# Optimization experiments

Measured on AMD Instinct MI355X. Metric: run time of the kernel, lower is better.

The kernel has to match this reference:

```python
import jax, jax.numpy as jnp
import numpy as np

N_NODES = 20000
DIM = 128
N_EDGES = 500000
BATCH = 16384
EPS = 1e-6  # torch.nn.PairwiseDistance default eps


def setup_inputs() -> dict:
    key = jax.random.key(0)
    k = jax.random.split(key, 8)
    edges = jax.random.randint(k[0], (2, N_EDGES), 0, N_NODES, dtype=jnp.int64 if jax.config.jax_enable_x64 else jnp.int32)
    nodes_p_star = jnp.sort(jax.random.randint(k[1], (BATCH,), 0, N_NODES))
    nodes_p = jnp.sort(jax.random.randint(k[2], (BATCH,), 0, N_NODES))
    # learned parameters, init in [-1, 1) as in the torch module
    beta_p = 2.0 * jax.random.uniform(k[3], (N_NODES,), dtype=jnp.float32) - 1.0
    beta_p_star = 2.0 * jax.random.uniform(k[4], (N_NODES,), dtype=jnp.float32) - 1.0
    p = 2.0 * jax.random.uniform(k[5], (N_NODES, DIM), dtype=jnp.float32) - 1.0
    p_star = 2.0 * jax.random.uniform(k[6], (N_NODES, DIM), dtype=jnp.float32) - 1.0
    return {
        "edges": edges,
        "nodes_p_star": nodes_p_star,
        "nodes_p": nodes_p,
        "beta_p": beta_p,
        "beta_p_star": beta_p_star,
        "p": p,
        "p_star": p_star,
    }


def reference(edges, nodes_p_star, nodes_p, beta_p, beta_p_star, p, p_star):
    # ---- link term: sum over observed edges of (beta - dist) ----
    beta_pair = beta_p_star[edges[0]] + beta_p[edges[1]]  # [E]
    diff = p[edges[0]] - p_star[edges[1]]                 # [E, D]
    # torch PairwiseDistance adds eps to the difference before the norm
    z_dist = jnp.sqrt(jnp.sum((diff + EPS) ** 2, axis=-1))
    link_term = jnp.sum(beta_pair - z_dist)

    # ---- non-link term: triu-masked sum of exp(beta - cdist) ----
    bps = beta_p_star[nodes_p_star]   # [Ns]
    bp = beta_p[nodes_p]              # [Np]
    ps = p_star[nodes_p_star]         # [Ns, D]
    pp = p[nodes_p]                   # [Np, D]
    beta_mat = bps[None, :] + bp[:, None]          # [Np, Ns]
    # cdist(ps, pp) -> [Ns, Np] via Gram trick
    sq = (jnp.sum(ps * ps, axis=-1)[:, None]
          + jnp.sum(pp * pp, axis=-1)[None, :]
          - 2.0 * jnp.einsum('nd,md->nm', ps, pp))
    dist_mat = jnp.sqrt(jnp.maximum(sq, 0.0))      # [Ns, Np]
    intensity = jnp.exp(beta_mat.T - dist_mat)     # [Ns, Np]
    non_link = jnp.sum(jnp.triu(intensity, k=1))

    return -(link_term - non_link)
```

## Files before the change

kernel.cpp:

```cpp
#include <hip/hip_runtime.h>

#define N_NODES 20000
#define DIM 128
#define N_EDGES 500000
#define BATCH 16384
#define EPS 1e-6f
#define L2E 1.4426950408889634f

typedef _Float16 half8 __attribute__((ext_vector_type(8)));
typedef _Float16 half4_t __attribute__((ext_vector_type(4)));
typedef float f32x4 __attribute__((ext_vector_type(4)));

__device__ __forceinline__ float fast_sqrtf(float x) {
#if __has_builtin(__builtin_amdgcn_sqrtf)
    return __builtin_amdgcn_sqrtf(x);
#else
    return sqrtf(x);
#endif
}
__device__ __forceinline__ float fast_exp2f(float x) {
#if __has_builtin(__builtin_amdgcn_exp2f)
    return __builtin_amdgcn_exp2f(x);
#else
    return exp2f(x);
#endif
}

#define NB_TILE 8256
#define N_BLK   512

#define OFF_PGEMM 0
#define OFF_PSH   33280
#define OFF_PPH   4227584
#define OFF_N2S   8421888
#define OFF_N2P   8487424
#define OFF_BPS   8552960
#define OFF_BP    8618496
#define OFF_END   8684032

__global__ __launch_bounds__(256) void prep_kernel(
    const float* __restrict__ p, const float* __restrict__ p_star,
    const float* __restrict__ beta_p, const float* __restrict__ beta_ps,
    const int* __restrict__ nodes_ps, const int* __restrict__ nodes_p,
    _Float16* __restrict__ Ah, float* __restrict__ n2A, float* __restrict__ bA2,
    _Float16* __restrict__ Bh, float* __restrict__ n2B, float* __restrict__ bB2)
{
    const int bx = blockIdx.x;
    const int g = threadIdx.x & 31;
    const int r8 = threadIdx.x >> 5;
    const bool isA = bx < 2048;
    const int row = (isA ? bx : bx - 2048) * 8 + r8;
    const int id = isA ? nodes_ps[row] : nodes_p[row];
    const float* src = isA ? p_star : p;
    float4 v = ((const float4*)(src + (size_t)id * DIM))[g];
    half4_t o;
    o[0] = (_Float16)v.x; o[1] = (_Float16)v.y; o[2] = (_Float16)v.z; o[3] = (_Float16)v.w;
    const int h = g >> 4;
    const int pc = ((g >> 1) & 7) ^ (row & 7);
    _Float16* dst = isA ? Ah : Bh;
    *(half4_t*)(dst + (size_t)row * DIM + (((h << 3) | pc) << 3) + (g & 1) * 4) = o;
    float nrm = v.x * v.x + v.y * v.y + v.z * v.z + v.w * v.w;
    #pragma unroll
    for (int m = 16; m >= 1; m >>= 1) nrm += __shfl_xor(nrm, m, 32);
    if (g == 0) {
        if (isA) { n2A[row] = nrm; bA2[row] = L2E * beta_ps[id]; }
        else     { n2B[row] = nrm; bB2[row] = L2E * beta_p[id]; }
    }
}

__device__ __forceinline__ void tile_of(int t, int& i0, int& j0, bool& diag) {
    const int by = t / 129;
    const int bx = t - by * 129;
    const int len = 128 - by;
    int ti, tj;
    if (bx < len) { ti = by; tj = by + bx; }
    else          { ti = 127 - by; tj = 127 - (bx - len); }
    i0 = ti << 7; j0 = tj << 7; diag = (ti == tj);
}

#define STAGE(I0, J0)                                                              \
    {                                                                              \
        _Pragma("unroll")                                                          \
        for (int u = 0; u < 4; ++u) {                                              \
            const int cidx = u * 512 + tid;                                        \
            const int row = cidx >> 4, cc = cidx & 15;                             \
            const int ldsoff = (u * 512 + w * 64) * 16;                            \
            __builtin_amdgcn_global_load_lds(                                      \
                (const __attribute__((address_space(1))) void*)(gA +               \
                    (((size_t)((I0) + row)) << 8) + (cc << 4)),                    \
                (__attribute__((address_space(3))) void*)(ldsA + ldsoff), 16, 0, 0); \
            __builtin_amdgcn_global_load_lds(                                      \
                (const __attribute__((address_space(1))) void*)(gB +               \
                    (((size_t)((J0) + row)) << 8) + (cc << 4)),                    \
                (__attribute__((address_space(3))) void*)(ldsB + ldsoff), 16, 0, 0); \
        }                                                                          \
    }

__global__ __launch_bounds__(512, 4) void main_kernel(
    const _Float16* __restrict__ Ag, const _Float16* __restrict__ Bg,
    const float* __restrict__ n2A, const float* __restrict__ n2B,
    const float* __restrict__ bA2, const float* __restrict__ bB2,
    const int* __restrict__ edges,
    const float* __restrict__ beta_p, const float* __restrict__ beta_ps,
    const float* __restrict__ pf, const float* __restrict__ psf,
    float* __restrict__ pgemm)
{
    __shared__ __align__(16) _Float16 As[128 * 128];
    __shared__ __align__(16) _Float16 Bs[128 * 128];
    __shared__ float smr[8];

    const int b = blockIdx.x;
    const int tid = threadIdx.x;
    const int lane = tid & 63;
    const int w = tid >> 6;
    const int wm = w & 3;
    const int wn = w >> 2;
    const int quad = lane >> 4;
    const int lr = lane & 15;
    const int k7 = lr & 7;

    auto* ldsA = (__attribute__((address_space(3))) char*)As;
    auto* ldsB = (__attribute__((address_space(3))) char*)Bs;
    const auto* gA = (const __attribute__((address_space(1))) char*)Ag;
    const auto* gB = (const __attribute__((address_space(1))) char*)Bg;

    float lsum = 0.f;

    int t = b;
    int i0, j0; bool diag;
    tile_of(t, i0, j0, diag);
    STAGE(i0, j0)
    __syncthreads();

    for (;;) {
        int cls = 0;
        if (diag) cls = (wn == 0) ? (wm >= 2 ? 2 : 1) : (wm >= 2 ? 1 : 0);

        f32x4 acc[2][4] = {};
        if (cls != 2) {
            #pragma unroll
            for (int ks = 0; ks < 4; ++ks) {
                const int lc = ks * 4 + quad;
                const int pcx = ((lc & 8) | ((lc & 7) ^ k7)) << 3;
                half8 af[2], bf[4];
                #pragma unroll
                for (int u = 0; u < 2; ++u)
                    af[u] = *(const half8*)&As[(wm * 32 + u * 16 + lr) * 128 + pcx];
                #pragma unroll
                for (int v = 0; v < 4; ++v)
                    bf[v] = *(const half8*)&Bs[(wn * 64 + v * 16 + lr) * 128 + pcx];
                #pragma unroll
                for (int mi = 0; mi < 2; ++mi)
                    #pragma unroll
                    for (int ni = 0; ni < 4; ++ni)
                        acc[mi][ni] = __builtin_amdgcn_mfma_f32_16x16x32_f16(
                            af[mi], bf[ni], acc[mi][ni], 0, 0, 0);
            }
        }

        const int ilo = i0 + wm * 32, jlo = j0 + wn * 64;
        const int tcur = t;
        __syncthreads();

        t += N_BLK;
        const bool more = (t < NB_TILE);
        if (more) {
            tile_of(t, i0, j0, diag);
            STAGE(i0, j0)
        }

        #pragma unroll
        for (int tt = 0; tt < 2; ++tt) {
            int e = tcur * 64 + w * 8 + quad * 2 + tt;
            if (e < N_EDGES) {
                int e0 = edges[e];
                int e1 = edges[N_EDGES + e];
                const float* ar = pf + (size_t)e0 * DIM + lr * 8;
                const float* br = psf + (size_t)e1 * DIM + lr * 8;
                f32x4 a0 = *(const f32x4*)ar;   f32x4 a1 = *(const f32x4*)(ar + 4);
                f32x4 b0 = *(const f32x4*)br;   f32x4 b1 = *(const f32x4*)(br + 4);
                float eb2 = (lr == 0) ? (beta_ps[e0] + beta_p[e1]) : 0.f;
                float s = 0.f;
                #pragma unroll
                for (int k = 0; k < 4; ++k) { float d = a0[k] - b0[k] + EPS; s = fmaf(d, d, s); }
                #pragma unroll
                for (int k = 0; k < 4; ++k) { float d = a1[k] - b1[k] + EPS; s = fmaf(d, d, s); }
                #pragma unroll
                for (int m = 8; m >= 1; m >>= 1) s += __shfl_xor(s, m, 16);
                if (lr == 0) lsum -= eb2 - fast_sqrtf(s);
            }
        }

        if (cls != 2) {
            f32x4 n2i[2], bi[2];
            #pragma unroll
            for (int mi = 0; mi < 2; ++mi) {
                n2i[mi] = *(const f32x4*)&n2A[ilo + mi * 16 + quad * 4];
                bi[mi]  = *(const f32x4*)&bA2[ilo + mi * 16 + quad * 4];
            }
            float n2j[4], bj[4];
            #pragma unroll
            for (int ni = 0; ni < 4; ++ni) {
                n2j[ni] = n2B[jlo + ni * 16 + lr];
                bj[ni]  = bB2[jlo + ni * 16 + lr];
            }

            if (cls == 0) {
                #pragma unroll
                for (int mi = 0; mi < 2; ++mi)
                    #pragma unroll
                    for (int ni = 0; ni < 4; ++ni) {
                        f32x4 d = acc[mi][ni];
                        #pragma unroll
                        for (int r = 0; r < 4; ++r) {
                            float tt = n2i[mi][r] + n2j[ni];
                            float sq = fmaxf(fmaf(d[r], -2.f, tt), 0.f);
                            float arg = fmaf(fast_sqrtf(sq), -L2E, bi[mi][r] + bj[ni]);
                            lsum += fast_exp2f(arg);
                        }
                    }
            } else {
                #pragma unroll
                for (int mi = 0; mi < 2; ++mi)
                    #pragma unroll
                    for (int ni = 0; ni < 4; ++ni) {
                        f32x4 d = acc[mi][ni];
                        #pragma unroll
                        for (int r = 0; r < 4; ++r) {
                            int ig = ilo + mi * 16 + quad * 4 + r;
                            int jg = jlo + ni * 16 + lr;
                            float tt = n2i[mi][r] + n2j[ni];
                            float sq = fmaxf(fmaf(d[r], -2.f, tt), 0.f);
                            float arg = fmaf(fast_sqrtf(sq), -L2E, bi[mi][r] + bj[ni]);
                            float ex = fast_exp2f(arg);
                            if (jg > ig) lsum += ex;
                        }
                    }
            }
        }

        if (!more) break;
        __syncthreads();
    }

    #pragma unroll
    for (int m = 32; m >= 1; m >>= 1) lsum += __shfl_xor(lsum, m, 64);
    if (lane == 0) smr[w] = lsum;
    __syncthreads();
    if (tid == 0) {
        float s = 0.f;
        #pragma unroll
        for (int i = 0; i < 8; ++i) s += smr[i];
        pgemm[b] = s;
    }
}

__global__ __launch_bounds__(1024) void reduce_kernel(
    const float* __restrict__ pg, float* __restrict__ out)
{
    float s = 0.f;
    for (int k = threadIdx.x; k < N_BLK; k += 1024) s += pg[k];
    #pragma unroll
    for (int m = 32; m >= 1; m >>= 1) s += __shfl_xor(s, m, 64);
    __shared__ float sm[16];
    if ((threadIdx.x & 63) == 0) sm[threadIdx.x >> 6] = s;
    __syncthreads();
    if (threadIdx.x == 0) {
        float t = 0.f;
        #pragma unroll
        for (int i = 0; i < 16; ++i) t += sm[i];
        out[0] = t;
    }
}

extern "C" void kernel_launch(void* const* d_in, const int* in_sizes, int n_in,
                              void* d_out, int out_size, void* d_ws, size_t ws_size,
                              hipStream_t stream) {
    const int* edges = (const int*)d_in[0];
    const int* nodes_p_star = (const int*)d_in[1];
    const int* nodes_p = (const int*)d_in[2];
    const float* beta_p = (const float*)d_in[3];
    const float* beta_p_star = (const float*)d_in[4];
    const float* p = (const float*)d_in[5];
    const float* p_star = (const float*)d_in[6];

    char* ws = (char*)d_ws;
    float* pgemm = (float*)(ws + OFF_PGEMM);
    _Float16* psh = (_Float16*)(ws + OFF_PSH);
    _Float16* pph = (_Float16*)(ws + OFF_PPH);
    float* n2s = (float*)(ws + OFF_N2S);
    float* n2p = (float*)(ws + OFF_N2P);
    float* bps2 = (float*)(ws + OFF_BPS);
    float* bp2 = (float*)(ws + OFF_BP);

    prep_kernel<<<4096, 256, 0, stream>>>(
        p, p_star, beta_p, beta_p_star, nodes_p_star, nodes_p,
        psh, n2s, bps2, pph, n2p, bp2);

    main_kernel<<<N_BLK, 512, 0, stream>>>(
        psh, pph, n2s, n2p, bps2, bp2,
        edges, beta_p, beta_p_star, p, p_star,
        pgemm);

    reduce_kernel<<<1, 1024, 0, stream>>>(pgemm, (float*)d_out);
}
```

Measured before the change: 193.3 us.

## Assign contiguous tile ranges per block, reuse A tiles, fuse final reduction

Each block now processes a contiguous run of about 16 upper-triangular tiles instead of striding by the grid size. Consecutive tiles usually share the same row tile, so A is only restaged into LDS when the row changes. The LDS staging layout is reorganized into K-halves to match the swizzle, and the epilogue distance/beta math is vectorized. The separate reduce kernel is replaced by a last-block-done atomic counter, which is reset in the prep kernel, removing one launch at the cost of an atomic and extra synchronization.

```diff
diff --git a/kernel.cpp b/kernel.cpp
--- a/kernel.cpp
+++ b/kernel.cpp
@@ -30,6 +30,7 @@
 #define N_BLK   512
 
 #define OFF_PGEMM 0
+#define OFF_CTR   16384
 #define OFF_PSH   33280
 #define OFF_PPH   4227584
 #define OFF_N2S   8421888
@@ -43,8 +44,10 @@
     const float* __restrict__ beta_p, const float* __restrict__ beta_ps,
     const int* __restrict__ nodes_ps, const int* __restrict__ nodes_p,
     _Float16* __restrict__ Ah, float* __restrict__ n2A, float* __restrict__ bA2,
-    _Float16* __restrict__ Bh, float* __restrict__ n2B, float* __restrict__ bB2)
+    _Float16* __restrict__ Bh, float* __restrict__ n2B, float* __restrict__ bB2,
+    unsigned* __restrict__ ctr)
 {
+    if (blockIdx.x == 0 && threadIdx.x == 0) *ctr = 0u;
     const int bx = blockIdx.x;
     const int g = threadIdx.x & 31;
     const int r8 = threadIdx.x >> 5;
@@ -78,23 +81,23 @@
     i0 = ti << 7; j0 = tj << 7; diag = (ti == tj);
 }
 
-#define STAGE(I0, J0)                                                              \
+#define STAGE_ARR(BASE0, GSRC, LDSOFF)                                             \
     {                                                                              \
         _Pragma("unroll")                                                          \
         for (int u = 0; u < 4; ++u) {                                              \
-            const int cidx = u * 512 + tid;                                        \
-            const int row = cidx >> 4, cc = cidx & 15;                             \
-            const int ldsoff = (u * 512 + w * 64) * 16;                            \
+            const int g8 = u * 8 + w;                                   \
+            const int h = g8 >> 4, rg = g8 & 15;                                   \
             __builtin_amdgcn_global_load_lds(                                      \
-                (const __attribute__((address_space(1))) void*)(gA +               \
-                    (((size_t)((I0) + row)) << 8) + (cc << 4)),                    \
-                (__attribute__((address_space(3))) void*)(ldsA + ldsoff), 16, 0, 0); \
-            __builtin_amdgcn_global_load_lds(                                      \
-                (const __attribute__((address_space(1))) void*)(gB +               \
-                    (((size_t)((J0) + row)) << 8) + (cc << 4)),                    \
-                (__attribute__((address_space(3))) void*)(ldsB + ldsoff), 16, 0, 0); \
+                (const __attribute__((address_space(1))) void*)((GSRC) +           \
+                    (((size_t)((BASE0) + rg * 8 + (lane >> 3))) << 8)              \
+                    + (h << 7) + ((lane & 7) << 4)),                               \
+                (__attribute__((address_space(3))) void*)(lds + (LDSOFF)           \
+                    + h * 16384 + rg * 1024), 16, 0, 0);                           \
         }                                                                          \
     }
+
+#define STAGE_A(I0) STAGE_ARR(I0, gA, 0)
+#define STAGE_B(J0) STAGE_ARR(J0, gB, 32768)
 
 __global__ __launch_bounds__(512, 4) void main_kernel(
     const _Float16* __restrict__ Ag, const _Float16* __restrict__ Bg,
@@ -103,11 +106,12 @@
     const int* __restrict__ edges,
     const float* __restrict__ beta_p, const float* __restrict__ beta_ps,
     const float* __restrict__ pf, const float* __restrict__ psf,
-    float* __restrict__ pgemm)
+    float* __restrict__ pgemm, unsigned* __restrict__ ctr,
+    float* __restrict__ out)
 {
-    __shared__ __align__(16) _Float16 As[128 * 128];
-    __shared__ __align__(16) _Float16 Bs[128 * 128];
+    __shared__ __align__(16) _Float16 sm16[32768];
     __shared__ float smr[8];
+    __shared__ int lastflag;
 
     const int b = blockIdx.x;
     const int tid = threadIdx.x;
@@ -119,17 +123,20 @@
     const int lr = lane & 15;
     const int k7 = lr & 7;
 
-    auto* ldsA = (__attribute__((address_space(3))) char*)As;
-    auto* ldsB = (__attribute__((address_space(3))) char*)Bs;
+    auto* lds = (__attribute__((address_space(3))) char*)sm16;
     const auto* gA = (const __attribute__((address_space(1))) char*)Ag;
     const auto* gB = (const __attribute__((address_space(1))) char*)Bg;
 
     float lsum = 0.f;
 
-    int t = b;
+    const int start = b * 16 + (b < 64 ? b : 64);
+    const int tend = start + 16 + (b < 64 ? 1 : 0);
+
+    int t = start;
     int i0, j0; bool diag;
     tile_of(t, i0, j0, diag);
-    STAGE(i0, j0)
+    STAGE_A(i0)
+    STAGE_B(j0)
     __syncthreads();
 
     for (;;) {
@@ -140,15 +147,16 @@
         if (cls != 2) {
             #pragma unroll
             for (int ks = 0; ks < 4; ++ks) {
-                const int lc = ks * 4 + quad;
-                const int pcx = ((lc & 8) | ((lc & 7) ^ k7)) << 3;
+                const int h = ks >> 1;
+                const int pc = (((ks & 1) << 2) | quad) ^ k7;
+                const int hb = h * 8192;
                 half8 af[2], bf[4];
                 #pragma unroll
                 for (int u = 0; u < 2; ++u)
-                    af[u] = *(const half8*)&As[(wm * 32 + u * 16 + lr) * 128 + pcx];
+                    af[u] = *(const half8*)&sm16[hb + (wm * 32 + u * 16 + lr) * 64 + pc * 8];
                 #pragma unroll
                 for (int v = 0; v < 4; ++v)
-                    bf[v] = *(const half8*)&Bs[(wn * 64 + v * 16 + lr) * 128 + pcx];
+                    bf[v] = *(const half8*)&sm16[16384 + hb + (wn * 64 + v * 16 + lr) * 64 + pc * 8];
                 #pragma unroll
                 for (int mi = 0; mi < 2; ++mi)
                     #pragma unroll
@@ -162,11 +170,13 @@
         const int tcur = t;
         __syncthreads();
 
-        t += N_BLK;
-        const bool more = (t < NB_TILE);
+        t += 1;
+        const bool more = (t < tend);
         if (more) {
+            const int pi0 = i0;
             tile_of(t, i0, j0, diag);
-            STAGE(i0, j0)
+            if (i0 != pi0) STAGE_A(i0)
+            STAGE_B(j0)
         }
 
         #pragma unroll
@@ -211,11 +221,13 @@
                     #pragma unroll
                     for (int ni = 0; ni < 4; ++ni) {
                         f32x4 d = acc[mi][ni];
+                        f32x4 ttv = n2i[mi] + n2j[ni];
+                        f32x4 sq = d * -2.0f + ttv;
+                        f32x4 bs = bi[mi] + bj[ni];
                         #pragma unroll
                         for (int r = 0; r < 4; ++r) {
-                            float tt = n2i[mi][r] + n2j[ni];
-                            float sq = fmaxf(fmaf(d[r], -2.f, tt), 0.f);
-                            float arg = fmaf(fast_sqrtf(sq), -L2E, bi[mi][r] + bj[ni]);
+                            float m0 = fmaxf(sq[r], 0.f);
+                            float arg = fmaf(fast_sqrtf(m0), -L2E, bs[r]);
                             lsum += fast_exp2f(arg);
                         }
                     }
@@ -225,13 +237,15 @@
                     #pragma unroll
                     for (int ni = 0; ni < 4; ++ni) {
                         f32x4 d = acc[mi][ni];
+                        f32x4 ttv = n2i[mi] + n2j[ni];
+                        f32x4 sq = d * -2.0f + ttv;
+                        f32x4 bs = bi[mi] + bj[ni];
                         #pragma unroll
                         for (int r = 0; r < 4; ++r) {
                             int ig = ilo + mi * 16 + quad * 4 + r;
                             int jg = jlo + ni * 16 + lr;
-                            float tt = n2i[mi][r] + n2j[ni];
-                            float sq = fmaxf(fmaf(d[r], -2.f, tt), 0.f);
-                            float arg = fmaf(fast_sqrtf(sq), -L2E, bi[mi][r] + bj[ni]);
+                            float m0 = fmaxf(sq[r], 0.f);
+                            float arg = fmaf(fast_sqrtf(m0), -L2E, bs[r]);
                             float ex = fast_exp2f(arg);
                             if (jg > ig) lsum += ex;
                         }
@@ -252,24 +266,25 @@
         #pragma unroll
         for (int i = 0; i < 8; ++i) s += smr[i];
         pgemm[b] = s;
-    }
-}
-
-__global__ __launch_bounds__(1024) void reduce_kernel(
-    const float* __restrict__ pg, float* __restrict__ out)
-{
-    float s = 0.f;
-    for (int k = threadIdx.x; k < N_BLK; k += 1024) s += pg[k];
-    #pragma unroll
-    for (int m = 32; m >= 1; m >>= 1) s += __shfl_xor(s, m, 64);
-    __shared__ float sm[16];
-    if ((threadIdx.x & 63) == 0) sm[threadIdx.x >> 6] = s;
+        unsigned prev = __hip_atomic_fetch_add(ctr, 1u, __ATOMIC_ACQ_REL,
+                                               __HIP_MEMORY_SCOPE_AGENT);
+        lastflag = (prev == N_BLK - 1) ? 1 : 0;
+    }
     __syncthreads();
-    if (threadIdx.x == 0) {
-        float t = 0.f;
+
+    if (lastflag) {
+        float s = __hip_atomic_load(&pgemm[tid], __ATOMIC_RELAXED,
+                                    __HIP_MEMORY_SCOPE_AGENT);
         #pragma unroll
-        for (int i = 0; i < 16; ++i) t += sm[i];
-        out[0] = t;
+        for (int m = 32; m >= 1; m >>= 1) s += __shfl_xor(s, m, 64);
+        if (lane == 0) smr[w] = s;
+        __syncthreads();
+        if (tid == 0) {
+            float tsum = 0.f;
+            #pragma unroll
+            for (int i = 0; i < 8; ++i) tsum += smr[i];
+            out[0] = tsum;
+        }
     }
 }
 
@@ -286,6 +301,7 @@
 
     char* ws = (char*)d_ws;
     float* pgemm = (float*)(ws + OFF_PGEMM);
+    unsigned* ctr = (unsigned*)(ws + OFF_CTR);
     _Float16* psh = (_Float16*)(ws + OFF_PSH);
     _Float16* pph = (_Float16*)(ws + OFF_PPH);
     float* n2s = (float*)(ws + OFF_N2S);
@@ -295,12 +311,10 @@
 
     prep_kernel<<<4096, 256, 0, stream>>>(
         p, p_star, beta_p, beta_p_star, nodes_p_star, nodes_p,
-        psh, n2s, bps2, pph, n2p, bp2);
+        psh, n2s, bps2, pph, n2p, bp2, ctr);
 
     main_kernel<<<N_BLK, 512, 0, stream>>>(
         psh, pph, n2s, n2p, bps2, bp2,
         edges, beta_p, beta_p_star, p, p_star,
-        pgemm);
-
-    reduce_kernel<<<1, 1024, 0, stream>>>(pgemm, (float*)d_out);
-}
+        pgemm, ctr, (float*)d_out);
+}
```

New measurement: 194.4 us. About the same (+0.5%).
